# Performance work log

Hardware: AMD Instinct MI355X
Metric: run time of the kernel (lower is better)

Reference implementation:

```python
import jax, jax.numpy as jnp
import numpy as np
import math

PHI = (1.0 + math.sqrt(5.0)) / 2.0
V, D, L, N, H = 50257, 128, 2, 512, 8
DH = D // H
B, S = 2, 256


def setup_inputs() -> dict:
    key = jax.random.key(0)
    ks = jax.random.split(key, 16)
    lim = 0.5 * math.sqrt(6.0 / (N + D))  # xavier_uniform gain=0.5 for Linear(N->D)
    return {
        "tokens": jax.random.randint(ks[0], (B, S), 0, V),
        "emb": (jax.random.normal(ks[1], (V, 2 * D)) * 0.02) * 0.5,
        "wq": jax.random.normal(ks[2], (L, H, DH)) * 0.02,
        "bq": jnp.zeros((L, H, DH)),
        "wk": jax.random.normal(ks[3], (L, H, DH)) * 0.02,
        "bk": jnp.zeros((L, H, DH)),
        "w_out": jax.random.normal(ks[4], (L, D)) * 0.02,
        "b_out": jnp.zeros((L, D)),
        "out_scale": jnp.ones((L, D)) * 0.5,
        "Wf": jax.random.normal(ks[5], (L, N, D)) * 0.02,
        "Bf": jnp.zeros((L, N, D)),
        "proj_real": jax.random.uniform(ks[6], (L, D, N), minval=-lim, maxval=lim),
        "proj_imag": jax.random.uniform(ks[7], (L, D, N), minval=-lim, maxval=lim),
        "attn_scale": jnp.ones((L,)),
        "res_scale": jnp.ones((L,)),
        "out_proj": jax.random.normal(ks[8], (V, D)) * 0.02,
    }


def reference(tokens, emb, wq, bq, wk, bk, w_out, b_out, out_scale, Wf, Bf,
              proj_real, proj_imag, attn_scale, res_scale, out_proj):
    dtype = emb.dtype
    wb = emb[tokens]                      # [B,S,2D] token -> (w, b) pairs
    w_e, b_e = wb[..., :D], wb[..., D:]
    t = jnp.arange(S, dtype=dtype)        # timestep per position

    # Recurrent Euler state evolution: theta = s/(1+|w|) + b + t*PHI ; s' = cos+sin
    def step(s, inp):
        w_t, b_t, tt = inp
        theta = s / (1.0 + jnp.abs(w_t)) + b_t + tt * PHI
        s_new = jnp.cos(theta) + jnp.sin(theta)
        return s_new, s_new

    _, states = jax.lax.scan(
        step, jnp.zeros((B, D), dtype),
        (jnp.moveaxis(w_e, 1, 0), jnp.moveaxis(b_e, 1, 0), t))
    states = jnp.moveaxis(states, 0, 1)   # [B,S,D] cached states

    causal = jnp.tril(jnp.ones((S, S), bool))  # cache includes current state
    t_phi = t * PHI
    scale = math.sqrt(2 * DH)

    x = states
    for l in range(L):
        # --- Euler attention ---
        xh = x.reshape(B, S, H, DH)
        th_q = xh / (1.0 + jnp.abs(wq[l])) + bq[l] + t_phi[None, :, None, None]
        q = jnp.concatenate([jnp.cos(th_q), jnp.sin(th_q)], axis=-1)  # [B,S,H,2DH]
        kh = states.reshape(B, S, H, DH)
        th_k = kh / (1.0 + jnp.abs(wk[l])) + bk[l]
        k = jnp.concatenate([jnp.cos(th_k), jnp.sin(th_k)], axis=-1)
        scores = jnp.einsum('bqhd,bkhd->bhqk', q, k) / scale
        scores = jnp.where(causal[None, None], scores, -jnp.inf)
        wts = jax.nn.softmax(scores, axis=-1)
        # each head attends over full-width cached states; heads are summed
        context = jnp.einsum('bhqk,bkd->bqd', wts, states)
        th_o = context / (1.0 + jnp.abs(w_out[l])) + b_out[l] + t_phi[None, :, None]
        attn_out = out_scale[l] * (jnp.cos(th_o) + jnp.sin(th_o))
        # --- Resonant FFN (per-neuron interference) ---
        th_f = x[:, :, None, :] / (1.0 + jnp.abs(Wf[l])) + Bf[l] + t[None, :, None, None]
        cos_sum = jnp.cos(th_f).sum(axis=-1)   # [B,S,N]
        sin_sum = jnp.sin(th_f).sum(axis=-1)
        res = cos_sum @ proj_real[l].T + sin_sum @ proj_imag[l].T
        res = jax.nn.silu(res)
        # additive fusion
        x = x + attn_scale[l] * attn_out + res_scale[l] * res

    logits = x @ out_proj.T                # [B,S,V]
    return logits
```

## Files before the change

### kernel.cpp

```cpp
#include <hip/hip_runtime.h>
#include <hip/hip_bf16.h>

using bf16x8 = __attribute__((ext_vector_type(8))) short;
using f32x4  = __attribute__((ext_vector_type(4))) float;

constexpr int cV  = 50257;
constexpr int cVp = 50688;
constexpr int cD  = 128;
constexpr int cN  = 512;
constexpr int cS  = 256;

#define PHI_F    1.6180339887498949f
#define INV2PI_F 0.15915494309189535f
#define SQRT2_F  1.4142135623730951f

__device__ __forceinline__ float fract1(float x) { return x - floorf(x); }

#if __has_builtin(__builtin_amdgcn_sinf)
__device__ __forceinline__ float sin_rev(float r) { return __builtin_amdgcn_sinf(r); }
__device__ __forceinline__ float cos_rev(float r) { return __builtin_amdgcn_cosf(r); }
#else
__device__ __forceinline__ float sin_rev(float r) { return __sinf(r * 6.2831853071795865f); }
__device__ __forceinline__ float cos_rev(float r) { return __cosf(r * 6.2831853071795865f); }
#endif

__device__ __forceinline__ unsigned short f2bf(float f) {
  unsigned u = __float_as_uint(f);
  unsigned r = (u + 0x7FFFu + ((u >> 16) & 1u)) >> 16;
  return (unsigned short)r;
}

__global__ void k_setup(const int* __restrict__ tokens, const float* __restrict__ emb,
                        float2* __restrict__ mc,
                        const float* __restrict__ pr, const float* __restrict__ pi,
                        float* __restrict__ pTR, float* __restrict__ pTI,
                        const float* __restrict__ W, unsigned short* __restrict__ Wbf) {
  int blk = blockIdx.x;
  if (blk < 256) {
    int idx = blk * 256 + threadIdx.x;
    int t = idx & 255, s = idx >> 8;
    int b = t >> 7, d = t & 127;
    int tok = tokens[b * cS + s];
    float w  = emb[tok * (2 * cD) + d];
    float be = emb[tok * (2 * cD) + cD + d];
    float m2 = SQRT2_F * INV2PI_F / (1.f + fabsf(w));
    float c  = fmaf((float)s, PHI_F, be) * INV2PI_F + 0.125f;
    mc[idx] = make_float2(m2, c);
  } else if (blk < 768) {
    int idx = (blk - 256) * 256 + threadIdx.x;
    int l = idx >> 16, rem = idx & 65535;
    int n = rem >> 7, d = rem & 127;
    int src = (l * cD + d) * cN + n;
    pTR[idx] = pr[src];
    pTI[idx] = pi[src];
  } else {
    int idx = (blk - 768) * 256 + threadIdx.x;
    int row = idx >> 4, c0 = (idx & 15) * 8;
    ushort4 o0 = {0,0,0,0}, o1 = {0,0,0,0};
    if (row < cV) {
      float4 w0 = *(const float4*)(W + (size_t)row * cD + c0);
      float4 w1 = *(const float4*)(W + (size_t)row * cD + c0 + 4);
      o0 = { f2bf(w0.x), f2bf(w0.y), f2bf(w0.z), f2bf(w0.w) };
      o1 = { f2bf(w1.x), f2bf(w1.y), f2bf(w1.z), f2bf(w1.w) };
    }
    unsigned short* dst = Wbf + (size_t)row * cD + c0;
    *(ushort4*)dst = o0;
    *(ushort4*)(dst + 4) = o1;
  }
}

__global__ void k_scan(const float2* __restrict__ mc, float* __restrict__ states) {
  int t = threadIdx.x;
  int b = t >> 7, d = t & 127;
  float2 buf[8];
#pragma unroll
  for (int i = 0; i < 8; ++i) buf[i] = mc[i * 256 + t];
  float sv = 0.f;
  float* out = states + (b * cS) * cD + d;
#pragma unroll 8
  for (int s = 0; s < cS; ++s) {
    float2 v = buf[s & 7];
    if (s + 8 < cS) buf[s & 7] = mc[(s + 8) * 256 + t];
    float r = fmaf(sv, v.x, v.y);
    sv = sin_rev(fract1(r));
    out[s * cD] = sv * SQRT2_F;
  }
}

__global__ __launch_bounds__(512) void k_layer(const float* __restrict__ x, const float* __restrict__ states,
                                               const float* __restrict__ wq, const float* __restrict__ bq,
                                               const float* __restrict__ wk, const float* __restrict__ bk,
                                               const float* __restrict__ Wf, const float* __restrict__ Bf,
                                               float* __restrict__ ctx, float* __restrict__ U, float* __restrict__ Vv) {
  int blk = blockIdx.x;
  if (blk < 256) {
    __shared__ __align__(16) float qrow[2][256];
    __shared__ float Psum[2][256];
    __shared__ float redm[2][4], reds[2][4];
    __shared__ float cred[2][256];
    __shared__ __align__(16) float rkl[128], bkl[128];
    int b = blk >> 7, qp = blk & 127;
    int sub = threadIdx.x >> 8;
    int t = threadIdx.x & 255;
    int q = qp * 2 + sub;
    if (threadIdx.x < 128) {
      int hd = threadIdx.x;
      rkl[hd] = INV2PI_F / (1.f + fabsf(wk[hd]));
      bkl[hd] = bk[hd] * INV2PI_F;
    }
    if (t < 128) {
      int hd = t;
      float rq = 1.f / (1.f + fabsf(wq[hd]));
      float thq = fmaf(x[(b * cS + q) * cD + hd], rq, fmaf((float)q, PHI_F, bq[hd])) * INV2PI_F;
      float fq = fract1(thq);
      qrow[sub][hd]       = cos_rev(fq);
      qrow[sub][128 + hd] = sin_rev(fq);
    }
    Psum[sub][t] = 0.f;
    __syncthreads();
    bool act = (t <= q);
    float sc[8];
    const float4* Sr = (const float4*)(states + (b * cS + t) * cD);
#pragma unroll
    for (int h = 0; h < 8; ++h) {
      float sacc = 0.f;
#pragma unroll
      for (int j = 0; j < 4; ++j) {
        float4 sv4 = Sr[h * 4 + j];
        int hd = h * 16 + j * 4;
        float sva[4] = { sv4.x, sv4.y, sv4.z, sv4.w };
#pragma unroll
        for (int c = 0; c < 4; ++c) {
          float f = fract1(fmaf(sva[c], rkl[hd + c], bkl[hd + c]));
          float ck = cos_rev(f), sk = sin_rev(f);
          sacc = fmaf(qrow[sub][hd + c], ck, fmaf(qrow[sub][128 + hd + c], sk, sacc));
        }
      }
      sc[h] = act ? sacc * 0.17677669529663689f : -3.0e38f;
    }
    int wid = t >> 6;
    for (int h = 0; h < 8; ++h) {
      float v = sc[h];
#pragma unroll
      for (int off = 32; off; off >>= 1) v = fmaxf(v, __shfl_xor(v, off, 64));
      if ((t & 63) == 0) redm[sub][wid] = v;
      __syncthreads();
      float m = fmaxf(fmaxf(redm[sub][0], redm[sub][1]), fmaxf(redm[sub][2], redm[sub][3]));
      float p = act ? __expf(sc[h] - m) : 0.f;
      float ps = p;
#pragma unroll
      for (int off = 32; off; off >>= 1) ps += __shfl_xor(ps, off, 64);
      if ((t & 63) == 0) reds[sub][wid] = ps;
      __syncthreads();
      float tot = reds[sub][0] + reds[sub][1] + reds[sub][2] + reds[sub][3];
      Psum[sub][t] += p / tot;
    }
    __syncthreads();
    int d = t & 127, half = t >> 7;
    float acc = 0.f;
    int k0 = half * 128;
    int kend = min(k0 + 128, q + 1);
    for (int kk = k0; kk < kend; ++kk)
      acc = fmaf(Psum[sub][kk], states[(b * cS + kk) * cD + d], acc);
    cred[sub][t] = acc;
    __syncthreads();
    if (half == 0) ctx[(b * cS + q) * cD + d] = cred[sub][t] + cred[sub][t + 128];
  } else {
    int fblk = blk - 256;
    int ns = fblk & 15, tg = fblk >> 4;
    constexpr int P = 130;
    __shared__ __align__(16) float finv[32 * P];
    __shared__ __align__(16) float fb[32 * P];
    __shared__ __align__(16) float xl[32 * 128];
    int t = threadIdx.x;
#pragma unroll
    for (int i = 0; i < 8; ++i) {
      int idx = t + i * 512;
      int rl = idx >> 7, d = idx & 127;
      int g = (ns * 32 + rl) * cD + d;
      finv[rl * P + d] = INV2PI_F / (1.f + fabsf(Wf[g]));
      fb[rl * P + d]   = Bf[g] * INV2PI_F;
      xl[idx] = x[(tg * 32 + rl) * cD + d];
    }
    __syncthreads();
    int nl = t & 31, tli = t >> 5;
#pragma unroll
    for (int p = 0; p < 2; ++p) {
      int tl = p * 16 + tli;
      int T = tg * 32 + tl;
      float srev = (float)(T & 255) * INV2PI_F;
      float uc = 0.f, us = 0.f;
      const float* fi  = finv + nl * P;
      const float* fbp = fb + nl * P;
      const float* xr  = xl + tl * 128;
#pragma unroll 4
      for (int d = 0; d < cD; d += 2) {
        float2 fiv = *(const float2*)(fi + d);
        float2 fbv = *(const float2*)(fbp + d);
        float2 xv  = *(const float2*)(xr + d);
        float f0 = fract1(fmaf(xv.x, fiv.x, fbv.x) + srev);
        float f1 = fract1(fmaf(xv.y, fiv.y, fbv.y) + srev);
        uc += cos_rev(f0);
        us += sin_rev(f0);
        uc += cos_rev(f1);
        us += sin_rev(f1);
      }
      U[T * cN + ns * 32 + nl]  = uc;
      Vv[T * cN + ns * 32 + nl] = us;
    }
  }
}

__global__ __launch_bounds__(512) void k_res(const float* __restrict__ U, const float* __restrict__ Vv,
                                             const float* __restrict__ pTR, const float* __restrict__ pTI,
                                             const float* __restrict__ ctx, const float* __restrict__ x,
                                             const float* __restrict__ w_out, const float* __restrict__ b_out,
                                             const float* __restrict__ out_scale,
                                             const float* __restrict__ attn_scale, const float* __restrict__ res_scale,
                                             int l, float* __restrict__ xout, unsigned short* __restrict__ xbf) {
  int blk = blockIdx.x;
  int t = threadIdx.x;
  __shared__ __align__(16) float uvU[4][512], uvV[4][512];
  __shared__ __align__(16) float4 part[3][4][32];
#pragma unroll
  for (int i = 0; i < 4; ++i) {
    int idx = t + i * 512;
    int tok = idx >> 9, n = idx & 511;
    uvU[tok][n] = U[(blk * 4 + tok) * cN + n];
    uvV[tok][n] = Vv[(blk * 4 + tok) * cN + n];
  }
  __syncthreads();
  int d4 = t & 31, tok = (t >> 5) & 3, nh = t >> 7;
  int T = blk * 4 + tok, s = T & 255;
  float a0 = 0.f, a1 = 0.f, a2 = 0.f, a3 = 0.f;
  const float* prB = pTR + (size_t)(l * cN) * cD + d4 * 4;
  const float* piB = pTI + (size_t)(l * cN) * cD + d4 * 4;
  int n0 = nh * 128;
#pragma unroll 4
  for (int n = n0; n < n0 + 128; ++n) {
    float4 pr = *(const float4*)(prB + n * cD);
    float4 pi = *(const float4*)(piB + n * cD);
    float wr = uvU[tok][n], wi = uvV[tok][n];
    a0 = fmaf(wr, pr.x, fmaf(wi, pi.x, a0));
    a1 = fmaf(wr, pr.y, fmaf(wi, pi.y, a1));
    a2 = fmaf(wr, pr.z, fmaf(wi, pi.z, a2));
    a3 = fmaf(wr, pr.w, fmaf(wi, pi.w, a3));
  }
  if (nh > 0) part[nh - 1][tok][d4] = make_float4(a0, a1, a2, a3);
  __syncthreads();
  if (nh == 0) {
    float rr[4] = { a0, a1, a2, a3 };
#pragma unroll
    for (int j = 0; j < 3; ++j) {
      float4 p = part[j][tok][d4];
      rr[0] += p.x; rr[1] += p.y; rr[2] += p.z; rr[3] += p.w;
    }
    int di = d4 * 4;
    float4 cx  = *(const float4*)(ctx + T * cD + di);
    float4 wo  = *(const float4*)(w_out + l * cD + di);
    float4 bo  = *(const float4*)(b_out + l * cD + di);
    float4 osc = *(const float4*)(out_scale + l * cD + di);
    float4 xv  = *(const float4*)(x + T * cD + di);
    float as = attn_scale[l], rs = res_scale[l];
    float sphi = (float)s * PHI_F;
    float cxa[4] = { cx.x, cx.y, cx.z, cx.w };
    float woa[4] = { wo.x, wo.y, wo.z, wo.w };
    float boa[4] = { bo.x, bo.y, bo.z, bo.w };
    float osa[4] = { osc.x, osc.y, osc.z, osc.w };
    float xva[4] = { xv.x, xv.y, xv.z, xv.w };
    float oa[4];
#pragma unroll
    for (int c = 0; c < 4; ++c) {
      float th = fmaf(cxa[c], 1.f / (1.f + fabsf(woa[c])), boa[c]) + sphi;
      float f = fract1(th * INV2PI_F);
      float ao = osa[c] * (cos_rev(f) + sin_rev(f));
      float r = rr[c];
      float sil = r / (1.f + __expf(-r));
      oa[c] = fmaf(as, ao, fmaf(rs, sil, xva[c]));
    }
    *(float4*)(xout + T * cD + di) = make_float4(oa[0], oa[1], oa[2], oa[3]);
    if (xbf) {
      ushort4 b4 = { f2bf(oa[0]), f2bf(oa[1]), f2bf(oa[2]), f2bf(oa[3]) };
      *(ushort4*)(xbf + T * cD + di) = b4;
    }
  }
}

__global__ __launch_bounds__(256) void k_gemm(const unsigned short* __restrict__ Xbf,
                                              const unsigned short* __restrict__ Wbf,
                                              float* __restrict__ out) {
  __shared__ __align__(16) float Cst[4][16 * 132];
  int t = threadIdx.x;
  int mchunk = blockIdx.x / 99, vchunk = blockIdx.x % 99;
  int m0 = mchunk * 64;
  int v0 = vchunk * 512;
  int wid = t >> 6, lane = t & 63, lr = lane & 15, lk = lane >> 4;
  int wv = wid * 128;
  const bf16x8* Xp = (const bf16x8*)Xbf;
  const bf16x8* Wp = (const bf16x8*)Wbf;
  f32x4 acc[4][8];
#pragma unroll
  for (int fm = 0; fm < 4; ++fm)
#pragma unroll
    for (int fv = 0; fv < 8; ++fv) acc[fm][fv] = (f32x4){0.f, 0.f, 0.f, 0.f};
#pragma unroll
  for (int ks = 0; ks < 4; ++ks) {
    bf16x8 a[4];
#pragma unroll
    for (int fm = 0; fm < 4; ++fm)
      a[fm] = Xp[(m0 + fm * 16 + lr) * 16 + ks * 4 + lk];
#pragma unroll
    for (int fv = 0; fv < 8; ++fv) {
      bf16x8 b = Wp[(size_t)(v0 + wv + fv * 16 + lr) * 16 + ks * 4 + lk];
#pragma unroll
      for (int fm = 0; fm < 4; ++fm)
        acc[fm][fv] = __builtin_amdgcn_mfma_f32_16x16x32_bf16(a[fm], b, acc[fm][fv], 0, 0, 0);
    }
  }
  float* Cp = &Cst[wid][0];
  int row2b = lane >> 5;
  int colg  = (lane & 31) * 4;
#pragma unroll
  for (int fm = 0; fm < 4; ++fm) {
#pragma unroll
    for (int fv = 0; fv < 8; ++fv)
#pragma unroll
      for (int r = 0; r < 4; ++r)
        Cp[(lk * 4 + r) * 132 + fv * 16 + lr] = acc[fm][fv][r];
#pragma unroll
    for (int step = 0; step < 8; ++step) {
      int rowl = step * 2 + row2b;
      float4 cv = *(const float4*)&Cp[rowl * 132 + colg];
      size_t rb = (size_t)(m0 + fm * 16 + rowl) * cV;
      int cb = v0 + wv + colg;
      if (cb + 3 < cV) {
        *(float4*)(out + rb + cb) = cv;
      } else {
        float ca[4] = { cv.x, cv.y, cv.z, cv.w };
#pragma unroll
        for (int j = 0; j < 4; ++j)
          if (cb + j < cV) out[rb + cb + j] = ca[j];
      }
    }
  }
}

extern "C" void kernel_launch(void* const* d_in, const int* in_sizes, int n_in,
                              void* d_out, int out_size, void* d_ws, size_t ws_size,
                              hipStream_t stream) {
  const int*   tokens    = (const int*)d_in[0];
  const float* emb       = (const float*)d_in[1];
  const float* wq        = (const float*)d_in[2];
  const float* bq        = (const float*)d_in[3];
  const float* wk        = (const float*)d_in[4];
  const float* bk        = (const float*)d_in[5];
  const float* w_out     = (const float*)d_in[6];
  const float* b_out     = (const float*)d_in[7];
  const float* out_scale = (const float*)d_in[8];
  const float* Wf        = (const float*)d_in[9];
  const float* Bf        = (const float*)d_in[10];
  const float* pr        = (const float*)d_in[11];
  const float* pi        = (const float*)d_in[12];
  const float* attn_s    = (const float*)d_in[13];
  const float* res_s     = (const float*)d_in[14];
  const float* out_proj  = (const float*)d_in[15];
  float* out = (float*)d_out;
  float* ws  = (float*)d_ws;

  float*  states = ws;
  float*  x1     = ws + 65536;
  float*  x2     = ws + 131072;
  float*  ctx    = ws + 196608;
  float2* mc     = (float2*)(ws + 262144);
  float*  U      = ws + 393216;
  float*  Vv     = ws + 655360;
  float*  pTR    = ws + 917504;
  float*  pTI    = ws + 1048576;
  unsigned short* X2bf = (unsigned short*)(ws + 1179648);
  unsigned short* Wbf  = (unsigned short*)(ws + 1212416);

  k_setup<<<768 + (cVp * 16) / 256, 256, 0, stream>>>(tokens, emb, mc, pr, pi, pTR, pTI,
                                                      out_proj, Wbf);
  k_scan<<<1, 256, 0, stream>>>(mc, states);

  const float* xin = states;
  float* xouts[2] = { x1, x2 };
  for (int l = 0; l < 2; ++l) {
    k_layer<<<512, 512, 0, stream>>>(xin, states, wq + l * 128, bq + l * 128,
                                     wk + l * 128, bk + l * 128,
                                     Wf + l * 65536, Bf + l * 65536, ctx, U, Vv);
    k_res<<<128, 512, 0, stream>>>(U, Vv, pTR, pTI, ctx, xin, w_out, b_out, out_scale,
                                   attn_s, res_s, l, xouts[l],
                                   (l == 1) ? X2bf : (unsigned short*)nullptr);
    xin = xouts[l];
  }
  k_gemm<<<8 * 99, 256, 0, stream>>>(X2bf, Wbf, out);
}
```

Before: 177.4 us.

## Swap MFMA operands in logits GEMM to store directly without LDS staging

The output-projection GEMM now passes the vocab weights as the A operand and activations as B, so each lane's accumulator holds four consecutive vocab columns. Those can be written straight to global memory as float4, which removes the LDS transpose buffer and its extra shared-memory traffic. The tiling becomes 16 rows by 2048 vocab columns per block, with 32 accumulators per wave, and the padded vocab size grows to 51200. In exchange, each weight tile is reused across fewer rows, so weights are re-read by all 32 row-chunks. Global stores now cover only 16 bytes per row per lane rather than fully coalesced rows.

```diff
diff --git a/kernel.cpp b/kernel.cpp
--- a/kernel.cpp
+++ b/kernel.cpp
@@ -5,7 +5,7 @@
 using f32x4  = __attribute__((ext_vector_type(4))) float;
 
 constexpr int cV  = 50257;
-constexpr int cVp = 50688;
+constexpr int cVp = 51200;
 constexpr int cD  = 128;
 constexpr int cN  = 512;
 constexpr int cS  = 256;
@@ -289,58 +289,36 @@
 __global__ __launch_bounds__(256) void k_gemm(const unsigned short* __restrict__ Xbf,
                                               const unsigned short* __restrict__ Wbf,
                                               float* __restrict__ out) {
-  __shared__ __align__(16) float Cst[4][16 * 132];
   int t = threadIdx.x;
-  int mchunk = blockIdx.x / 99, vchunk = blockIdx.x % 99;
-  int m0 = mchunk * 64;
-  int v0 = vchunk * 512;
+  int vchunk = blockIdx.x >> 5, mchunk = blockIdx.x & 31;
+  int m0 = mchunk * 16;
+  int v0 = vchunk * 2048;
   int wid = t >> 6, lane = t & 63, lr = lane & 15, lk = lane >> 4;
-  int wv = wid * 128;
+  int vw = v0 + wid * 512;
   const bf16x8* Xp = (const bf16x8*)Xbf;
   const bf16x8* Wp = (const bf16x8*)Wbf;
-  f32x4 acc[4][8];
-#pragma unroll
-  for (int fm = 0; fm < 4; ++fm)
-#pragma unroll
-    for (int fv = 0; fv < 8; ++fv) acc[fm][fv] = (f32x4){0.f, 0.f, 0.f, 0.f};
+  f32x4 acc[32];
+#pragma unroll
+  for (int fv = 0; fv < 32; ++fv) acc[fv] = (f32x4){0.f, 0.f, 0.f, 0.f};
 #pragma unroll
   for (int ks = 0; ks < 4; ++ks) {
-    bf16x8 a[4];
-#pragma unroll
-    for (int fm = 0; fm < 4; ++fm)
-      a[fm] = Xp[(m0 + fm * 16 + lr) * 16 + ks * 4 + lk];
-#pragma unroll
-    for (int fv = 0; fv < 8; ++fv) {
-      bf16x8 b = Wp[(size_t)(v0 + wv + fv * 16 + lr) * 16 + ks * 4 + lk];
-#pragma unroll
-      for (int fm = 0; fm < 4; ++fm)
-        acc[fm][fv] = __builtin_amdgcn_mfma_f32_16x16x32_bf16(a[fm], b, acc[fm][fv], 0, 0, 0);
-    }
-  }
-  float* Cp = &Cst[wid][0];
-  int row2b = lane >> 5;
-  int colg  = (lane & 31) * 4;
-#pragma unroll
-  for (int fm = 0; fm < 4; ++fm) {
-#pragma unroll
-    for (int fv = 0; fv < 8; ++fv)
-#pragma unroll
-      for (int r = 0; r < 4; ++r)
-        Cp[(lk * 4 + r) * 132 + fv * 16 + lr] = acc[fm][fv][r];
-#pragma unroll
-    for (int step = 0; step < 8; ++step) {
-      int rowl = step * 2 + row2b;
-      float4 cv = *(const float4*)&Cp[rowl * 132 + colg];
-      size_t rb = (size_t)(m0 + fm * 16 + rowl) * cV;
-      int cb = v0 + wv + colg;
-      if (cb + 3 < cV) {
-        *(float4*)(out + rb + cb) = cv;
-      } else {
-        float ca[4] = { cv.x, cv.y, cv.z, cv.w };
-#pragma unroll
-        for (int j = 0; j < 4; ++j)
-          if (cb + j < cV) out[rb + cb + j] = ca[j];
-      }
+    bf16x8 bX = Xp[(m0 + lr) * 16 + ks * 4 + lk];
+#pragma unroll
+    for (int fv = 0; fv < 32; ++fv) {
+      bf16x8 aW = Wp[(size_t)(vw + fv * 16 + lr) * 16 + ks * 4 + lk];
+      acc[fv] = __builtin_amdgcn_mfma_f32_16x16x32_bf16(aW, bX, acc[fv], 0, 0, 0);
+    }
+  }
+  size_t rb = (size_t)(m0 + lr) * cV;
+#pragma unroll
+  for (int fv = 0; fv < 32; ++fv) {
+    int cb = vw + fv * 16 + lk * 4;
+    if (cb + 3 < cV) {
+      *(f32x4*)(out + rb + cb) = acc[fv];
+    } else {
+#pragma unroll
+      for (int j = 0; j < 4; ++j)
+        if (cb + j < cV) out[rb + cb + j] = acc[fv][j];
     }
   }
 }
@@ -394,5 +372,5 @@
                                    (l == 1) ? X2bf : (unsigned short*)nullptr);
     xin = xouts[l];
   }
-  k_gemm<<<8 * 99, 256, 0, stream>>>(X2bf, Wbf, out);
-}
+  k_gemm<<<25 * 32, 256, 0, stream>>>(X2bf, Wbf, out);
+}
```

Measured after the change: 221.7 us. +25.0%, slower.
